# Kernel optimization log

Measured on AMD Instinct MI355X. Metric: run time of the kernel, lower is better.

The kernel has to match this reference:

```python
import jax, jax.numpy as jnp
import numpy as np

EMB = 384
HID = 256
HEADS = 4
HD = HID // HEADS  # 64
LAYERS = 2
M_DOCS = 32
TOTAL = 4096  # 1 query + 32 docs + 4063 sentences
LN_EPS = 1e-5


def _layernorm(x, scale, bias):
    mu = jnp.mean(x, axis=-1, keepdims=True)
    var = jnp.mean(jnp.square(x - mu), axis=-1, keepdims=True)
    return (x - mu) * jax.lax.rsqrt(var + LN_EPS) * scale + bias


def setup_inputs() -> dict:
    key = jax.random.key(0)
    ks = jax.random.split(key, 12)
    g = 0.05  # small init scale (stand-in for xavier)
    return {
        "node_embeddings": jax.random.normal(ks[0], (TOTAL, EMB), jnp.float32),
        "adj": jax.random.randint(ks[1], (TOTAL, TOTAL), 0, 2, jnp.int32),
        "num_docs": M_DOCS,
        "proj_w": jax.random.normal(ks[2], (HID, EMB), jnp.float32) * g,
        "proj_b": jnp.zeros((HID,), jnp.float32),
        "ln_scale": jnp.ones((LAYERS, HID), jnp.float32),
        "ln_bias": jnp.zeros((LAYERS, HID), jnp.float32),
        "gat_W": jax.random.normal(ks[3], (LAYERS, HEADS, HD, HID), jnp.float32) * g,
        "gat_a": jax.random.normal(ks[4], (LAYERS, HEADS, 2 * HD), jnp.float32) * g,
        "fusion_w": jax.random.normal(ks[5], (HID, 2 * HID + 2), jnp.float32) * g,
        "fusion_b": jnp.zeros((HID,), jnp.float32),
        "out_w": jax.random.normal(ks[6], (HID,), jnp.float32) * g,
        "out_b": jnp.float32(0.5),
    }


def reference(node_embeddings, adj, num_docs, proj_w, proj_b, ln_scale, ln_bias,
              gat_W, gat_a, fusion_w, fusion_b, out_w, out_b):
    T = node_embeddings.shape[0]
    M = num_docs
    N = T - 1 - M  # number of sentences
    # input projection + relu (dropout = identity in eval)
    h = jax.nn.relu(node_embeddings @ proj_w.T + proj_b)  # (T, HID)
    # query-guided sentence re-weighting
    q = h[0:1]                     # (1, HID)
    s = h[1 + M:]                  # (N, HID)
    qn = q / (jnp.linalg.norm(q, axis=1, keepdims=True) + 1e-8)
    sn = s / (jnp.linalg.norm(s, axis=1, keepdims=True) + 1e-8)
    cos = (qn @ sn.T).reshape(-1, 1)          # (N,1)
    s = s + 0.8 * q * cos
    h = jnp.concatenate([h[:1 + M], s], axis=0)
    mask = (adj == 0)[None]                   # (1,T,T)
    for i in range(LAYERS):
        res = h
        x = _layernorm(h, ln_scale[i], ln_bias[i])
        Wh = jnp.einsum('nd,hkd->hnk', x, gat_W[i])                # (H,T,HD)
        # concat-attention a.[Wh_i ; Wh_j] == a_src.Wh_i + a_dst.Wh_j
        src = jnp.einsum('hnk,hk->hn', Wh, gat_a[i, :, :HD])       # (H,T)
        dst = jnp.einsum('hnk,hk->hn', Wh, gat_a[i, :, HD:])       # (H,T)
        e = jax.nn.leaky_relu(src[:, :, None] + dst[:, None, :], 0.2)  # (H,T,T)
        e = jnp.where(mask, -jnp.inf, e)
        attn = jax.nn.softmax(e, axis=-1)                          # softmax over j
        hn = jnp.einsum('hij,hjk->hik', attn, Wh)                  # (H,T,HD)
        hcat = jnp.transpose(hn, (1, 0, 2)).reshape(T, HEADS * HD)
        h = 0.5 * jax.nn.relu(hcat) + 0.5 * res
    qh = h[0:1]
    sh = h[1 + M:]
    scores = (qh @ sh.T) / (HID ** 0.5)       # (1,N)
    aw = jax.nn.softmax(scores, axis=-1)
    awT = aw.T                                # (N,1)
    qw = qh * (awT + 0.5)                     # (N,HID)
    qnf = qh / (jnp.linalg.norm(qh, axis=1, keepdims=True) + 1e-8)
    snf = sh / (jnp.linalg.norm(sh, axis=1, keepdims=True) + 1e-8)
    cosf = (qnf @ snf.T).reshape(-1, 1)       # (N,1)
    feat = jnp.concatenate([sh, qw, cosf, awT], axis=1)  # (N, 2*HID+2)
    g = jax.nn.relu(feat @ fusion_w.T + fusion_b)
    out = g @ out_w + out_b                   # (N,)
    return out + 0.5 * cosf[:, 0]
```

## Files before the change

### kernel.cpp

```cpp
#include <hip/hip_runtime.h>
#include <hip/hip_bf16.h>
#include <stdint.h>

#define TOTAL 4096
#define EMB 384
#define MD 32
#define NDOCS (TOTAL - 1 - MD)
#define LN_EPS 1e-5f

typedef __hip_bfloat16 bf16;
typedef unsigned short ushort_t;
typedef __attribute__((ext_vector_type(8))) short short8;
typedef __attribute__((ext_vector_type(4))) float f32x4;
typedef __attribute__((ext_vector_type(2))) float f32x2;

__device__ __forceinline__ float ldf(const void* p, int i, int isbf) {
    return isbf ? __bfloat162float(((const bf16*)p)[i]) : ((const float*)p)[i];
}

__device__ __forceinline__ unsigned f2bf(float x) {
    return (__float_as_uint(x) + 0x8000u) >> 16;
}

__device__ __forceinline__ unsigned fenc(float f) {
    unsigned u = __float_as_uint(f);
    return (u >> 31) ? ~u : (u | 0x80000000u);
}
__device__ __forceinline__ float fdec(unsigned k) {
    return __uint_as_float((k & 0x80000000u) ? (k & 0x7FFFFFFFu) : ~k);
}

#define NTRANS ((EMB * 256 + 2 * 65536 + 514 * 256) / 256)
__global__ void k_adjmask(const int* adj, unsigned long long* maskb,
                          const uint16_t* embp, int* flag, unsigned* dmaxu,
                          const void* proj_w, const void* gat_W, const void* fusion_w,
                          float* projT, float* gatT, float* fwT) {
    __shared__ int red[4];
    int i = blockIdx.x, t = threadIdx.x;
    int w = t >> 6, l = t & 63;
    for (int c = w; c < 64; c += 4) {
        int a = adj[(size_t)i * TOTAL + c * 64 + l];
        unsigned long long m = __ballot(a != 0);
        if (l == 0) maskb[i * 64 + c] = m;
    }
    if (i == 0) {
        for (int idx = t; idx < 2048; idx += 256) dmaxu[idx] = 0x007FFFFFu;
    }
    if (i < NTRANS) {
        int cnt = 0;
        for (int k = t; k < 4096; k += 256) {
            uint16_t wd = embp[2 * k];
            int e = (wd >> 7) & 0xFF;
            if (e >= 100 && e <= 140) cnt++;
        }
        for (int o = 32; o > 0; o >>= 1) cnt += __shfl_down(cnt, o);
        if ((t & 63) == 0) red[t >> 6] = cnt;
        __syncthreads();
        int isbf = (red[0] + red[1] + red[2] + red[3] > 2048) ? 1 : 0;
        if (i == 0 && t == 0) flag[0] = isbf;
        int idx = i * 256 + t;
        if (idx < EMB * 256) {
            int d = idx >> 8, c = idx & 255;
            projT[idx] = ldf(proj_w, c * EMB + d, isbf);
        } else if (idx < EMB * 256 + 2 * 65536) {
            int r = idx - EMB * 256;
            int ll = r >> 16, rem = r & 65535;
            int d = rem >> 8, c = rem & 255;
            gatT[r] = ldf(gat_W, ll * 65536 + c * 256 + d, isbf);
        } else {
            int r = idx - (EMB * 256 + 2 * 65536);
            int j = r >> 8, c = r & 255;
            fwT[r] = ldf(fusion_w, c * 514 + j, isbf);
        }
    }
}

#define PR 8
__global__ void k_proj(const void* emb, const void* proj_b, const float* projT, float* h,
                       const int* flagp) {
    __shared__ float xs[PR][EMB];
    int isbf = flagp[0];
    int i0 = blockIdx.x * PR, t = threadIdx.x;
    for (int idx = t; idx < PR * EMB; idx += 256) {
        int r = idx / EMB, d = idx % EMB;
        xs[r][d] = ldf(emb, (i0 + r) * EMB + d, isbf);
    }
    __syncthreads();
    float acc[PR];
    float bias = ldf(proj_b, t, isbf);
#pragma unroll
    for (int r = 0; r < PR; r++) acc[r] = bias;
    for (int d0 = 0; d0 < EMB; d0 += 4) {
        float w0 = projT[d0 * 256 + t];
        float w1 = projT[(d0 + 1) * 256 + t];
        float w2 = projT[(d0 + 2) * 256 + t];
        float w3 = projT[(d0 + 3) * 256 + t];
#pragma unroll
        for (int r = 0; r < PR; r++) {
            float4 x = *(const float4*)&xs[r][d0];
            acc[r] = fmaf(x.x, w0, acc[r]);
            acc[r] = fmaf(x.y, w1, acc[r]);
            acc[r] = fmaf(x.z, w2, acc[r]);
            acc[r] = fmaf(x.w, w3, acc[r]);
        }
    }
#pragma unroll
    for (int r = 0; r < PR; r++) h[(size_t)(i0 + r) * 256 + t] = fmaxf(acc[r], 0.f);
}

#define LR 8
__global__ void k_ln_wh(float* h, const float* gatT, const void* ln_scale,
                        const void* ln_bias, const void* gat_a,
                        ushort_t* whswz, float* srcb, unsigned* d12g, unsigned* dmaxu,
                        const float* hnp, const float* lpart, int layer, int doepi,
                        const int* flagp) {
    __shared__ float xs[LR][256];
    __shared__ float red[2][LR][4];
    __shared__ float qsm[256];
    __shared__ float qred[4];
    int isbf = flagp[0];
    int i0 = blockIdx.x * LR, t = threadIdx.x;
    int w = t >> 6, l = t & 63;
    float scale = ldf(ln_scale, layer * 256 + t, isbf);
    float bias = ldf(ln_bias, layer * 256 + t, isbf);
    float hv[LR];
    if (doepi) {
#pragma unroll
        for (int r = 0; r < LR; r++) {
            int i = i0 + r;
            float lsum = lpart[(size_t)w * 4096 + i] + lpart[(size_t)(4 + w) * 4096 + i] +
                         lpart[(size_t)(8 + w) * 4096 + i] + lpart[(size_t)(12 + w) * 4096 + i];
            float s = hnp[(size_t)i * 256 + t] + hnp[(size_t)TOTAL * 256 + i * 256 + t] +
                      hnp[(size_t)2 * TOTAL * 256 + i * 256 + t] +
                      hnp[(size_t)3 * TOTAL * 256 + i * 256 + t];
            float hn = 0.5f * fmaxf(s / lsum, 0.f) + 0.5f * h[(size_t)i * 256 + t];
            hv[r] = hn;
            h[(size_t)i * 256 + t] = hn;
        }
    } else {
        qsm[t] = h[t];
#pragma unroll
        for (int r = 0; r < LR; r++) hv[r] = h[(size_t)(i0 + r) * 256 + t];
        __syncthreads();
        float qv = qsm[t];
        {
            float a = qv * qv;
            for (int o = 32; o > 0; o >>= 1) a += __shfl_down(a, o);
            if (l == 0) qred[w] = a;
        }
#pragma unroll
        for (int r = 0; r < LR; r++) {
            float b = hv[r] * hv[r], c = qv * hv[r];
            for (int o = 32; o > 0; o >>= 1) { b += __shfl_down(b, o); c += __shfl_down(c, o); }
            if (l == 0) { red[0][r][w] = b; red[1][r][w] = c; }
        }
        __syncthreads();
        if (i0 + LR > 1 + MD) {
            float qn = sqrtf(qred[0] + qred[1] + qred[2] + qred[3]) + 1e-8f;
#pragma unroll
            for (int r = 0; r < LR; r++) {
                int i = i0 + r;
                if (i >= 1 + MD) {
                    float bs = red[0][r][0] + red[0][r][1] + red[0][r][2] + red[0][r][3];
                    float cs = red[1][r][0] + red[1][r][1] + red[1][r][2] + red[1][r][3];
                    float k = 0.8f * (cs / (qn * (sqrtf(bs) + 1e-8f)));
                    hv[r] += k * qv;
                    h[(size_t)i * 256 + t] = hv[r];
                }
            }
        }
        __syncthreads();
    }
#pragma unroll
    for (int r = 0; r < LR; r++) {
        float a = hv[r], b = hv[r] * hv[r];
        for (int o = 32; o > 0; o >>= 1) { a += __shfl_down(a, o); b += __shfl_down(b, o); }
        if (l == 0) { red[0][r][w] = a; red[1][r][w] = b; }
    }
    __syncthreads();
#pragma unroll
    for (int r = 0; r < LR; r++) {
        float mu = (red[0][r][0] + red[0][r][1] + red[0][r][2] + red[0][r][3]) * (1.f / 256.f);
        float var = (red[1][r][0] + red[1][r][1] + red[1][r][2] + red[1][r][3]) * (1.f / 256.f) - mu * mu;
        float x = (hv[r] - mu) * rsqrtf(var + LN_EPS) * scale + bias;
        xs[r][t] = x;
    }
    __syncthreads();
    const float* gT = gatT + layer * 65536;
    float acc[LR];
#pragma unroll
    for (int r = 0; r < LR; r++) acc[r] = 0.f;
    for (int d0 = 0; d0 < 256; d0 += 4) {
        float w0 = gT[d0 * 256 + t];
        float w1 = gT[(d0 + 1) * 256 + t];
        float w2 = gT[(d0 + 2) * 256 + t];
        float w3 = gT[(d0 + 3) * 256 + t];
#pragma unroll
        for (int r = 0; r < LR; r++) {
            float4 x = *(const float4*)&xs[r][d0];
            acc[r] = fmaf(x.x, w0, acc[r]);
            acc[r] = fmaf(x.y, w1, acc[r]);
            acc[r] = fmaf(x.z, w2, acc[r]);
            acc[r] = fmaf(x.w, w3, acc[r]);
        }
    }
    float av1 = ldf(gat_a, layer * 512 + w * 128 + l, isbf);
    float av2 = ldf(gat_a, layer * 512 + w * 128 + 64 + l, isbf);
    const float LOG2E = 1.44269504f;
    float mmax = -__builtin_inff();
#pragma unroll
    for (int r = 0; r < LR; r++) {
        int i = i0 + r;
        int off = (i >> 6) * 16384 + (t >> 6) * 4096 + ((i >> 3) & 7) * 512 +
                  ((t >> 4) & 3) * 128 + (t & 15) * 8 + (i & 7);
        whswz[off] = (ushort_t)f2bf(acc[r]);
        float sv = acc[r] * av1, dv = acc[r] * av2;
        for (int o = 32; o > 0; o >>= 1) { sv += __shfl_down(sv, o); dv += __shfl_down(dv, o); }
        if (l == 0) {
            srcb[w * 4096 + i] = sv;
            float D1 = exp2f(dv * LOG2E), D2 = exp2f(0.2f * dv * LOG2E);
            d12g[w * 4096 + i] = (f2bf(D2) << 16) | f2bf(D1);
            mmax = fmaxf(mmax, dv);
        }
    }
    if (l == 0) atomicMax(&dmaxu[(blockIdx.x & 63) * 16 + w], fenc(mmax));
}

#define TI 32
#define JS 4
__global__ __launch_bounds__(512) void k_pv(const ushort_t* whswz, const float* srcb,
                                            const unsigned* dmaxu, const unsigned* d12g,
                                            const unsigned long long* maskb,
                                            float* hnp, float* lpart) {
    __shared__ __align__(16) char smem[32768];
    __shared__ __align__(16) float lsh[4][2][4][4];
    __shared__ unsigned mlut[4];
    __shared__ float dmx[4];
    unsigned* d12s = (unsigned*)smem;
    unsigned long long* mbs = (unsigned long long*)(smem + 16384);
    float* srcs = (float*)(smem + 16384 + 4352);
    f32x4* accsh = (f32x4*)smem;
    int t = threadIdx.x;
    int W = t >> 6, lane = t & 63;
    int h = W & 3, kq = W >> 2;
    int quad = lane >> 4, c16 = lane & 15;
    int i0 = blockIdx.x * TI;
    int jbase = blockIdx.y * 1024;
    if (t < 4) mlut[t] = (t & 1 ? 0x0000FFFFu : 0u) | (t & 2 ? 0xFFFF0000u : 0u);
    if (t < 256) {
        int hh = t >> 6, sl = t & 63;
        float v = fdec(dmaxu[sl * 16 + hh]);
        for (int o = 32; o > 0; o >>= 1) v = fmaxf(v, __shfl_xor(v, o));
        if (sl == 0) dmx[hh] = v;
    }
    for (int idx = t; idx < TI * 16; idx += 512) {
        int r = idx >> 4, wd = idx & 15;
        mbs[r * 17 + wd] = maskb[(size_t)(i0 + r) * 64 + (jbase >> 6) + wd];
    }
    for (int idx = t; idx < 1024; idx += 512) {
        int hh = idx >> 8, j4 = idx & 255;
        ((uint4*)d12s)[idx] = ((const uint4*)(d12g + hh * 4096 + jbase))[j4];
    }
    if (t < 128) {
        int h2 = t >> 5, r = t & 31;
        srcs[h2 * 32 + r] = srcb[h2 * 4096 + i0 + r];
    }
    __syncthreads();
    const float LOG2E = 1.44269504f;
    float dm = dmx[h];
    float E1[2], E2[2];
#pragma unroll
    for (int rt = 0; rt < 2; rt++) {
        float src = srcs[h * 32 + rt * 16 + c16];
        float sd = src + dm;
        float rce = -fmaxf(sd, 0.2f * sd);
        E1[rt] = exp2f((src + rce) * LOG2E);
        E2[rt] = exp2f((0.2f * src + rce) * LOG2E);
    }
    f32x4 acc[2][4];
    f32x4 accl[2] = {(f32x4){0.f, 0.f, 0.f, 0.f}, (f32x4){0.f, 0.f, 0.f, 0.f}};
#pragma unroll
    for (int rt = 0; rt < 2; rt++)
#pragma unroll
        for (int ct = 0; ct < 4; ct++) acc[rt][ct] = (f32x4){0.f, 0.f, 0.f, 0.f};
    uint4 onesu;
    unsigned os = (c16 == 0) ? 0x3F803F80u : 0u;
    onesu.x = os; onesu.y = os; onesu.z = os; onesu.w = os;
    short8 bfones = __builtin_bit_cast(short8, onesu);
    const uint4* g4 = (const uint4*)whswz;
    size_t b0 = (size_t)(jbase >> 6) * 2048 + h * 512 + (kq * 4 + quad) * 64 + c16;
    uint4 bn[4];
#pragma unroll
    for (int ct = 0; ct < 4; ct++) bn[ct] = g4[b0 + ct * 16];
    for (int step = 0; step < 16; step++) {
        uint4 bc[4];
#pragma unroll
        for (int ct = 0; ct < 4; ct++) bc[ct] = bn[ct];
        if (step < 15) {
            size_t bs = b0 + (size_t)(step + 1) * 2048;
#pragma unroll
            for (int ct = 0; ct < 4; ct++) bn[ct] = g4[bs + ct * 16];
        }
        int jl0 = step * 64 + kq * 32 + quad * 8;
        unsigned mby[2];
#pragma unroll
        for (int rt = 0; rt < 2; rt++)
            mby[rt] = (unsigned)(mbs[(rt * 16 + c16) * 17 + step] >> (kq * 32 + quad * 8)) & 0xFFu;
        const uint4* dj = (const uint4*)&d12s[h * 1024 + jl0];
        uint4 da = dj[0], db = dj[1];
        unsigned dw[8] = {da.x, da.y, da.z, da.w, db.x, db.y, db.z, db.w};
        f32x2 D1[4], D2[4];
#pragma unroll
        for (int q = 0; q < 4; q++) {
            unsigned a = dw[2 * q], b = dw[2 * q + 1];
            D1[q] = (f32x2){__uint_as_float(a << 16), __uint_as_float(b << 16)};
            D2[q] = (f32x2){__uint_as_float(a & 0xFFFF0000u), __uint_as_float(b & 0xFFFF0000u)};
        }
        uint4 afu[2];
#pragma unroll
        for (int rt = 0; rt < 2; rt++) {
            unsigned pu[4];
#pragma unroll
            for (int q = 0; q < 4; q++) {
                f32x2 v1 = D1[q] * E1[rt];
                f32x2 v2 = D2[q] * E2[rt];
                f32x2 m = __builtin_elementwise_max(v1, v2);
                unsigned v = ((__float_as_uint(m.x) + 0x8000u) >> 16) |
                             ((__float_as_uint(m.y) + 0x8000u) & 0xFFFF0000u);
                pu[q] = v & mlut[(mby[rt] >> (2 * q)) & 3u];
            }
            afu[rt].x = pu[0]; afu[rt].y = pu[1]; afu[rt].z = pu[2]; afu[rt].w = pu[3];
        }
        short8 af0 = __builtin_bit_cast(short8, afu[0]);
        short8 af1 = __builtin_bit_cast(short8, afu[1]);
#pragma unroll
        for (int ct = 0; ct < 4; ct++) {
            short8 bf = __builtin_bit_cast(short8, bc[ct]);
            acc[0][ct] = __builtin_amdgcn_mfma_f32_16x16x32_bf16(af0, bf, acc[0][ct], 0, 0, 0);
            acc[1][ct] = __builtin_amdgcn_mfma_f32_16x16x32_bf16(af1, bf, acc[1][ct], 0, 0, 0);
        }
        accl[0] = __builtin_amdgcn_mfma_f32_16x16x32_bf16(af0, bfones, accl[0], 0, 0, 0);
        accl[1] = __builtin_amdgcn_mfma_f32_16x16x32_bf16(af1, bfones, accl[1], 0, 0, 0);
    }
    __syncthreads();
    if (kq == 1) {
#pragma unroll
        for (int rt = 0; rt < 2; rt++) {
#pragma unroll
            for (int ct = 0; ct < 4; ct++)
                accsh[((h * 2 + rt) * 4 + ct) * 64 + lane] = acc[rt][ct];
            if (c16 == 0) *(f32x4*)&lsh[h][rt][quad][0] = accl[rt];
        }
    }
    __syncthreads();
    if (kq == 0) {
        float* out = hnp + (size_t)blockIdx.y * (TOTAL * 256);
#pragma unroll
        for (int rt = 0; rt < 2; rt++) {
#pragma unroll
            for (int ct = 0; ct < 4; ct++) {
                f32x4 o = acc[rt][ct] + accsh[((h * 2 + rt) * 4 + ct) * 64 + lane];
#pragma unroll
                for (int rr = 0; rr < 4; rr++) {
                    int row = i0 + rt * 16 + quad * 4 + rr;
                    out[(size_t)row * 256 + h * 64 + ct * 16 + c16] = o[rr];
                }
            }
            if (c16 == 0) {
                f32x4 lv = accl[rt] + *(const f32x4*)&lsh[h][rt][quad][0];
#pragma unroll
                for (int rr = 0; rr < 4; rr++)
                    lpart[(size_t)(blockIdx.y * 4 + h) * 4096 + i0 + rt * 16 + quad * 4 + rr] = lv[rr];
            }
        }
    }
}

__global__ __launch_bounds__(256) void k_scores(float* h, const float* hnp, const float* lpart,
                                                float* qrow, float* scoresv, float* cosv,
                                                float* swp) {
    int t = threadIdx.x, W = t >> 6, lane = t & 63;
    int hh = lane >> 4;
    float4* h4 = (float4*)h;
    const float4* p0 = (const float4*)hnp;
    const float4* p1 = p0 + (size_t)TOTAL * 64;
    const float4* p2 = p1 + (size_t)TOTAL * 64;
    const float4* p3 = p2 + (size_t)TOTAL * 64;
    int gw = blockIdx.x * 4 + W;
    float lq = lpart[(size_t)hh * 4096] + lpart[(size_t)(4 + hh) * 4096] +
               lpart[(size_t)(8 + hh) * 4096] + lpart[(size_t)(12 + hh) * 4096];
    float4 a0 = p0[lane], a1 = p1[lane], a2 = p2[lane], a3 = p3[lane];
    float4 hq = h4[lane];
    float invq = 1.f / lq;
    float4 q4;
    q4.x = 0.5f * fmaxf((a0.x + a1.x + a2.x + a3.x) * invq, 0.f) + 0.5f * hq.x;
    q4.y = 0.5f * fmaxf((a0.y + a1.y + a2.y + a3.y) * invq, 0.f) + 0.5f * hq.y;
    q4.z = 0.5f * fmaxf((a0.z + a1.z + a2.z + a3.z) * invq, 0.f) + 0.5f * hq.z;
    q4.w = 0.5f * fmaxf((a0.w + a1.w + a2.w + a3.w) * invq, 0.f) + 0.5f * hq.w;
    if (gw == 0) ((float4*)qrow)[lane] = q4;
    float a = q4.x * q4.x + q4.y * q4.y + q4.z * q4.z + q4.w * q4.w;
    for (int o = 32; o > 0; o >>= 1) a += __shfl_xor(a, o);
    float qn = sqrtf(a) + 1e-8f;
    float mw = -__builtin_inff(), sw = 0.f;
    for (int n = gw; n < NDOCS; n += 1024) {
        int row = 1 + MD + n;
        size_t ro = (size_t)row * 64;
        float ld = lpart[(size_t)hh * 4096 + row] + lpart[(size_t)(4 + hh) * 4096 + row] +
                   lpart[(size_t)(8 + hh) * 4096 + row] + lpart[(size_t)(12 + hh) * 4096 + row];
        float4 b0 = p0[ro + lane], b1 = p1[ro + lane], b2 = p2[ro + lane], b3 = p3[ro + lane];
        float4 ho = h4[ro + lane];
        float invd = 1.f / ld;
        float4 s4;
        s4.x = 0.5f * fmaxf((b0.x + b1.x + b2.x + b3.x) * invd, 0.f) + 0.5f * ho.x;
        s4.y = 0.5f * fmaxf((b0.y + b1.y + b2.y + b3.y) * invd, 0.f) + 0.5f * ho.y;
        s4.z = 0.5f * fmaxf((b0.z + b1.z + b2.z + b3.z) * invd, 0.f) + 0.5f * ho.z;
        s4.w = 0.5f * fmaxf((b0.w + b1.w + b2.w + b3.w) * invd, 0.f) + 0.5f * ho.w;
        h4[ro + lane] = s4;
        float b = s4.x * s4.x + s4.y * s4.y + s4.z * s4.z + s4.w * s4.w;
        float c = q4.x * s4.x + q4.y * s4.y + q4.z * s4.z + q4.w * s4.w;
        for (int o = 32; o > 0; o >>= 1) { b += __shfl_xor(b, o); c += __shfl_xor(c, o); }
        float sc = c * (1.f / 16.f);
        if (lane == 0) {
            scoresv[n] = sc;
            cosv[n] = c / (qn * (sqrtf(b) + 1e-8f));
        }
        float mn = fmaxf(mw, sc);
        sw = sw * __expf(mw - mn) + __expf(sc - mn);
        mw = mn;
    }
    if (lane == 0) { swp[2 * gw] = mw; swp[2 * gw + 1] = sw; }
}

#define TN 8
__global__ __launch_bounds__(256) void k_fusion(const float* h, const float* qrow,
                                                const float* scoresv, const float* swp,
                                                const float* cosv,
                                                const float* fwT, const void* fusion_b,
                                                const void* out_w, const void* out_bp,
                                                void* outv, const int* flagp) {
    __shared__ float feats2[514][TN];
    __shared__ float qhs[256];
    __shared__ float red[TN][4];
    __shared__ float reds[2][4];
    __shared__ float aws[TN];
    int isbf = flagp[0];
    int t = threadIdx.x;
    int n0 = blockIdx.x * TN;
    qhs[t] = qrow[t];
    float M = -__builtin_inff(), S = 0.f;
    for (int idx = t; idx < 1024; idx += 256) {
        float pm = swp[2 * idx], ps = swp[2 * idx + 1];
        float mn = fmaxf(M, pm);
        S = S * __expf(M - mn) + ps * __expf(pm - mn);
        M = mn;
    }
    for (int o = 32; o > 0; o >>= 1) {
        float m2 = __shfl_xor(M, o), s2 = __shfl_xor(S, o);
        float mn = fmaxf(M, m2);
        S = S * __expf(M - mn) + s2 * __expf(m2 - mn);
        M = mn;
    }
    if ((t & 63) == 0) { reds[0][t >> 6] = M; reds[1][t >> 6] = S; }
    __syncthreads();
    float Mf = fmaxf(fmaxf(reds[0][0], reds[0][1]), fmaxf(reds[0][2], reds[0][3]));
    float Sf = reds[1][0] * __expf(reds[0][0] - Mf) + reds[1][1] * __expf(reds[0][1] - Mf) +
               reds[1][2] * __expf(reds[0][2] - Mf) + reds[1][3] * __expf(reds[0][3] - Mf);
    float invS = 1.f / Sf;
    if (t < TN) {
        int n = n0 + t;
        aws[t] = (n < NDOCS) ? __expf(scoresv[n] - Mf) * invS : 0.f;
    }
    __syncthreads();
    for (int idx = t; idx < 514 * TN; idx += 256) {
        int j = idx >> 3, r = idx & 7;
        int n = n0 + r;
        float v = 0.f;
        if (n < NDOCS) {
            if (j < 256) v = h[(size_t)(1 + MD + n) * 256 + j];
            else if (j < 512) v = qhs[j - 256] * (aws[r] + 0.5f);
            else if (j == 512) v = cosv[n];
            else v = aws[r];
        }
        feats2[j][r] = v;
    }
    __syncthreads();
    float acc[TN];
    float bk = ldf(fusion_b, t, isbf);
#pragma unroll
    for (int r = 0; r < TN; r++) acc[r] = bk;
    for (int j0 = 0; j0 < 512; j0 += 8) {
        float wv[8];
#pragma unroll
        for (int u = 0; u < 8; u++) wv[u] = fwT[(j0 + u) * 256 + t];
#pragma unroll
        for (int u = 0; u < 8; u++) {
            float4 fa = *(const float4*)&feats2[j0 + u][0];
            float4 fb = *(const float4*)&feats2[j0 + u][4];
            acc[0] = fmaf(fa.x, wv[u], acc[0]); acc[1] = fmaf(fa.y, wv[u], acc[1]);
            acc[2] = fmaf(fa.z, wv[u], acc[2]); acc[3] = fmaf(fa.w, wv[u], acc[3]);
            acc[4] = fmaf(fb.x, wv[u], acc[4]); acc[5] = fmaf(fb.y, wv[u], acc[5]);
            acc[6] = fmaf(fb.z, wv[u], acc[6]); acc[7] = fmaf(fb.w, wv[u], acc[7]);
        }
    }
#pragma unroll
    for (int j = 512; j < 514; j++) {
        float wv = fwT[j * 256 + t];
#pragma unroll
        for (int r = 0; r < TN; r++) acc[r] = fmaf(feats2[j][r], wv, acc[r]);
    }
    float ow = ldf(out_w, t, isbf);
    float outb = ldf(out_bp, 0, isbf);
#pragma unroll
    for (int r = 0; r < TN; r++) {
        float o = fmaxf(acc[r], 0.f) * ow;
        for (int off = 32; off > 0; off >>= 1) o += __shfl_down(o, off);
        if ((t & 63) == 0) red[r][t >> 6] = o;
    }
    __syncthreads();
    if (t < TN) {
        int n = n0 + t;
        if (n < NDOCS) {
            float o = red[t][0] + red[t][1] + red[t][2] + red[t][3] + outb + 0.5f * cosv[n];
            if (isbf) ((bf16*)outv)[n] = __float2bfloat16(o);
            else      ((float*)outv)[n] = o;
        }
    }
}

extern "C" void kernel_launch(void* const* d_in, const int* in_sizes, int n_in,
                              void* d_out, int out_size, void* d_ws, size_t ws_size,
                              hipStream_t stream) {
    const void* emb      = d_in[0];
    const int*  adj      = (const int*)d_in[1];
    const void* proj_w   = d_in[3];
    const void* proj_b   = d_in[4];
    const void* ln_scale = d_in[5];
    const void* ln_bias  = d_in[6];
    const void* gat_W    = d_in[7];
    const void* gat_a    = d_in[8];
    const void* fusion_w = d_in[9];
    const void* fusion_b = d_in[10];
    const void* out_w    = d_in[11];
    const void* out_b    = d_in[12];

    unsigned long long* maskb = (unsigned long long*)d_ws;
    int* flag = (int*)((char*)d_ws + (size_t)4096 * 64 * 8);
    float* f = (float*)((char*)d_ws + (size_t)4096 * 64 * 8 + 256);
    float* h       = f; f += 4096 * 256;
    float* srcb    = f; f += 4 * 4096;
    unsigned* d12g = (unsigned*)f; f += 4 * 4096;
    unsigned* dmaxu = (unsigned*)f; f += 2048;
    float* projT   = f; f += EMB * 256;
    float* gatT    = f; f += 2 * 65536;
    float* fwT     = f; f += 514 * 256;
    float* scoresv = f; f += 4096;
    float* cosv    = f; f += 4096;
    float* swpart  = f; f += 4096;
    float* qrow    = f; f += 256;
    float* lpart   = f; f += 4 * 4 * 4096;
    ushort_t* whswz = (ushort_t*)f; f += 4096 * 256 / 2;
    float* hnp     = f; f += (size_t)JS * 4096 * 256;

    k_adjmask<<<dim3(4096), dim3(256), 0, stream>>>(adj, maskb, (const uint16_t*)emb, flag,
                                                    dmaxu, proj_w, gat_W, fusion_w,
                                                    projT, gatT, fwT);
    k_proj<<<dim3(TOTAL / PR), dim3(256), 0, stream>>>(emb, proj_b, projT, h, flag);
    for (int layer = 0; layer < 2; layer++) {
        k_ln_wh<<<dim3(TOTAL / LR), dim3(256), 0, stream>>>(h, gatT, ln_scale, ln_bias, gat_a,
                                                            whswz, srcb, d12g, dmaxu + layer * 1024,
                                                            hnp, lpart, layer, layer, flag);
        k_pv<<<dim3(TOTAL / TI, JS), dim3(512), 0, stream>>>(whswz, srcb, dmaxu + layer * 1024,
                                                             d12g, maskb, hnp, lpart);
    }
    k_scores<<<dim3(256), dim3(256), 0, stream>>>(h, hnp, lpart, qrow, scoresv, cosv, swpart);
    k_fusion<<<dim3((NDOCS + TN - 1) / TN), dim3(256), 0, stream>>>(h, qrow, scoresv, swpart,
                                                                    cosv, fwT, fusion_b, out_w,
                                                                    out_b, (void*)d_out, flag);
}
```

Baseline: 304.1 us.

## Fuse projection, GAT layers, scoring and fusion into one persistent kernel

Replaces the chain of seven kernel launches after the mask build with one persistent kernel of 512 blocks of 512 threads. The stages are separated by software grid barriers built from atomics, and dynamic shared memory is reused across stages. The aim is to remove launch overhead and inter-kernel gaps. In exchange, stages that used 256 threads leave half of each block idle, the barriers rely on all blocks being co-resident, and the spin loop has a timeout fallback that could break correctness.

```diff
diff --git a/kernel.cpp b/kernel.cpp
--- a/kernel.cpp
+++ b/kernel.cpp
@@ -7,6 +7,7 @@
 #define MD 32
 #define NDOCS (TOTAL - 1 - MD)
 #define LN_EPS 1e-5f
+#define NEGF (-1e30f)
 
 typedef __hip_bfloat16 bf16;
 typedef unsigned short ushort_t;
@@ -30,11 +31,30 @@
     return __uint_as_float((k & 0x80000000u) ? (k & 0x7FFFFFFFu) : ~k);
 }
 
+__device__ __forceinline__ void gsync(unsigned* bar) {
+    __syncthreads();
+    if (threadIdx.x == 0) {
+        __threadfence();
+        unsigned old = atomicAdd(bar, 1u);
+        if (old == 511u) {
+            __hip_atomic_store(bar + 32, 1u, __ATOMIC_RELEASE, __HIP_MEMORY_SCOPE_AGENT);
+        } else {
+            long long t0 = clock64();
+            while (__hip_atomic_load(bar + 32, __ATOMIC_ACQUIRE, __HIP_MEMORY_SCOPE_AGENT) == 0u) {
+                __builtin_amdgcn_s_sleep(8);
+                if (clock64() - t0 > 200000000LL) break;
+            }
+        }
+    }
+    __syncthreads();
+    __threadfence();
+}
+
 #define NTRANS ((EMB * 256 + 2 * 65536 + 514 * 256) / 256)
 __global__ void k_adjmask(const int* adj, unsigned long long* maskb,
                           const uint16_t* embp, int* flag, unsigned* dmaxu,
                           const void* proj_w, const void* gat_W, const void* fusion_w,
-                          float* projT, float* gatT, float* fwT) {
+                          float* projT, float* gatT, float* fwT, unsigned* gbar) {
     __shared__ int red[4];
     int i = blockIdx.x, t = threadIdx.x;
     int w = t >> 6, l = t & 63;
@@ -45,6 +65,7 @@
     }
     if (i == 0) {
         for (int idx = t; idx < 2048; idx += 256) dmaxu[idx] = 0x007FFFFFu;
+        for (int idx = t; idx < 384; idx += 256) gbar[idx] = 0u;
     }
     if (i < NTRANS) {
         int cnt = 0;
@@ -76,86 +97,101 @@
 }
 
 #define PR 8
-__global__ void k_proj(const void* emb, const void* proj_b, const float* projT, float* h,
-                       const int* flagp) {
-    __shared__ float xs[PR][EMB];
-    int isbf = flagp[0];
-    int i0 = blockIdx.x * PR, t = threadIdx.x;
-    for (int idx = t; idx < PR * EMB; idx += 256) {
-        int r = idx / EMB, d = idx % EMB;
-        xs[r][d] = ldf(emb, (i0 + r) * EMB + d, isbf);
-    }
-    __syncthreads();
-    float acc[PR];
-    float bias = ldf(proj_b, t, isbf);
-#pragma unroll
-    for (int r = 0; r < PR; r++) acc[r] = bias;
-    for (int d0 = 0; d0 < EMB; d0 += 4) {
-        float w0 = projT[d0 * 256 + t];
-        float w1 = projT[(d0 + 1) * 256 + t];
-        float w2 = projT[(d0 + 2) * 256 + t];
-        float w3 = projT[(d0 + 3) * 256 + t];
-#pragma unroll
-        for (int r = 0; r < PR; r++) {
-            float4 x = *(const float4*)&xs[r][d0];
-            acc[r] = fmaf(x.x, w0, acc[r]);
-            acc[r] = fmaf(x.y, w1, acc[r]);
-            acc[r] = fmaf(x.z, w2, acc[r]);
-            acc[r] = fmaf(x.w, w3, acc[r]);
-        }
-    }
-#pragma unroll
-    for (int r = 0; r < PR; r++) h[(size_t)(i0 + r) * 256 + t] = fmaxf(acc[r], 0.f);
+__device__ __forceinline__ void dev_proj(const void* emb, const void* proj_b,
+                                         const float* projT, float* h, int isbf, int bid) {
+    extern __shared__ char BIGDYN[];
+    float (*xs)[EMB] = (float (*)[EMB])BIGDYN;
+    int t5 = threadIdx.x;
+    bool act = t5 < 256;
+    int t = t5 & 255;
+    int i0 = bid * PR;
+    if (act) {
+        for (int idx = t; idx < PR * EMB; idx += 256) {
+            int r = idx / EMB, d = idx % EMB;
+            xs[r][d] = ldf(emb, (i0 + r) * EMB + d, isbf);
+        }
+    }
+    __syncthreads();
+    if (act) {
+        float acc[PR];
+        float bias = ldf(proj_b, t, isbf);
+#pragma unroll
+        for (int r = 0; r < PR; r++) acc[r] = bias;
+        for (int d0 = 0; d0 < EMB; d0 += 4) {
+            float w0 = projT[d0 * 256 + t];
+            float w1 = projT[(d0 + 1) * 256 + t];
+            float w2 = projT[(d0 + 2) * 256 + t];
+            float w3 = projT[(d0 + 3) * 256 + t];
+#pragma unroll
+            for (int r = 0; r < PR; r++) {
+                float4 x = *(const float4*)&xs[r][d0];
+                acc[r] = fmaf(x.x, w0, acc[r]);
+                acc[r] = fmaf(x.y, w1, acc[r]);
+                acc[r] = fmaf(x.z, w2, acc[r]);
+                acc[r] = fmaf(x.w, w3, acc[r]);
+            }
+        }
+#pragma unroll
+        for (int r = 0; r < PR; r++) h[(size_t)(i0 + r) * 256 + t] = fmaxf(acc[r], 0.f);
+    }
 }
 
 #define LR 8
-__global__ void k_ln_wh(float* h, const float* gatT, const void* ln_scale,
-                        const void* ln_bias, const void* gat_a,
-                        ushort_t* whswz, float* srcb, unsigned* d12g, unsigned* dmaxu,
-                        const float* hnp, const float* lpart, int layer, int doepi,
-                        const int* flagp) {
-    __shared__ float xs[LR][256];
+__device__ __forceinline__ void dev_ln(float* h, const float* gatT, const void* ln_scale,
+        const void* ln_bias, const void* gat_a, ushort_t* whswz, float* srcb,
+        unsigned* d12g, unsigned* dmaxu, const float* hnp, const float* lpart,
+        int layer, int doepi, int isbf, int bid) {
+    extern __shared__ char BIGDYN[];
+    float (*xs)[256] = (float (*)[256])BIGDYN;
     __shared__ float red[2][LR][4];
     __shared__ float qsm[256];
     __shared__ float qred[4];
-    int isbf = flagp[0];
-    int i0 = blockIdx.x * LR, t = threadIdx.x;
+    int t5 = threadIdx.x;
+    bool act = t5 < 256;
+    int t = t5 & 255;
     int w = t >> 6, l = t & 63;
+    int i0 = bid * LR;
     float scale = ldf(ln_scale, layer * 256 + t, isbf);
     float bias = ldf(ln_bias, layer * 256 + t, isbf);
     float hv[LR];
+#pragma unroll
+    for (int r = 0; r < LR; r++) hv[r] = 0.f;
     if (doepi) {
-#pragma unroll
-        for (int r = 0; r < LR; r++) {
-            int i = i0 + r;
-            float lsum = lpart[(size_t)w * 4096 + i] + lpart[(size_t)(4 + w) * 4096 + i] +
-                         lpart[(size_t)(8 + w) * 4096 + i] + lpart[(size_t)(12 + w) * 4096 + i];
-            float s = hnp[(size_t)i * 256 + t] + hnp[(size_t)TOTAL * 256 + i * 256 + t] +
-                      hnp[(size_t)2 * TOTAL * 256 + i * 256 + t] +
-                      hnp[(size_t)3 * TOTAL * 256 + i * 256 + t];
-            float hn = 0.5f * fmaxf(s / lsum, 0.f) + 0.5f * h[(size_t)i * 256 + t];
-            hv[r] = hn;
-            h[(size_t)i * 256 + t] = hn;
+        if (act) {
+#pragma unroll
+            for (int r = 0; r < LR; r++) {
+                int i = i0 + r;
+                float lsum = lpart[(size_t)w * 4096 + i] + lpart[(size_t)(4 + w) * 4096 + i] +
+                             lpart[(size_t)(8 + w) * 4096 + i] + lpart[(size_t)(12 + w) * 4096 + i];
+                float s = hnp[(size_t)i * 256 + t] + hnp[(size_t)TOTAL * 256 + i * 256 + t] +
+                          hnp[(size_t)2 * TOTAL * 256 + i * 256 + t] +
+                          hnp[(size_t)3 * TOTAL * 256 + i * 256 + t];
+                float hn = 0.5f * fmaxf(s / lsum, 0.f) + 0.5f * h[(size_t)i * 256 + t];
+                hv[r] = hn;
+                h[(size_t)i * 256 + t] = hn;
+            }
         }
     } else {
-        qsm[t] = h[t];
-#pragma unroll
-        for (int r = 0; r < LR; r++) hv[r] = h[(size_t)(i0 + r) * 256 + t];
+        if (act) {
+            qsm[t] = h[t];
+#pragma unroll
+            for (int r = 0; r < LR; r++) hv[r] = h[(size_t)(i0 + r) * 256 + t];
+        }
         __syncthreads();
         float qv = qsm[t];
-        {
+        if (act) {
             float a = qv * qv;
             for (int o = 32; o > 0; o >>= 1) a += __shfl_down(a, o);
             if (l == 0) qred[w] = a;
-        }
-#pragma unroll
-        for (int r = 0; r < LR; r++) {
-            float b = hv[r] * hv[r], c = qv * hv[r];
-            for (int o = 32; o > 0; o >>= 1) { b += __shfl_down(b, o); c += __shfl_down(c, o); }
-            if (l == 0) { red[0][r][w] = b; red[1][r][w] = c; }
+#pragma unroll
+            for (int r = 0; r < LR; r++) {
+                float b = hv[r] * hv[r], c = qv * hv[r];
+                for (int o = 32; o > 0; o >>= 1) { b += __shfl_down(b, o); c += __shfl_down(c, o); }
+                if (l == 0) { red[0][r][w] = b; red[1][r][w] = c; }
+            }
         }
         __syncthreads();
-        if (i0 + LR > 1 + MD) {
+        if (act && i0 + LR > 1 + MD) {
             float qn = sqrtf(qred[0] + qred[1] + qred[2] + qred[3]) + 1e-8f;
 #pragma unroll
             for (int r = 0; r < LR; r++) {
@@ -171,68 +207,75 @@
         }
         __syncthreads();
     }
-#pragma unroll
-    for (int r = 0; r < LR; r++) {
-        float a = hv[r], b = hv[r] * hv[r];
-        for (int o = 32; o > 0; o >>= 1) { a += __shfl_down(a, o); b += __shfl_down(b, o); }
-        if (l == 0) { red[0][r][w] = a; red[1][r][w] = b; }
-    }
-    __syncthreads();
-#pragma unroll
-    for (int r = 0; r < LR; r++) {
-        float mu = (red[0][r][0] + red[0][r][1] + red[0][r][2] + red[0][r][3]) * (1.f / 256.f);
-        float var = (red[1][r][0] + red[1][r][1] + red[1][r][2] + red[1][r][3]) * (1.f / 256.f) - mu * mu;
-        float x = (hv[r] - mu) * rsqrtf(var + LN_EPS) * scale + bias;
-        xs[r][t] = x;
-    }
-    __syncthreads();
-    const float* gT = gatT + layer * 65536;
-    float acc[LR];
-#pragma unroll
-    for (int r = 0; r < LR; r++) acc[r] = 0.f;
-    for (int d0 = 0; d0 < 256; d0 += 4) {
-        float w0 = gT[d0 * 256 + t];
-        float w1 = gT[(d0 + 1) * 256 + t];
-        float w2 = gT[(d0 + 2) * 256 + t];
-        float w3 = gT[(d0 + 3) * 256 + t];
+    if (act) {
 #pragma unroll
         for (int r = 0; r < LR; r++) {
-            float4 x = *(const float4*)&xs[r][d0];
-            acc[r] = fmaf(x.x, w0, acc[r]);
-            acc[r] = fmaf(x.y, w1, acc[r]);
-            acc[r] = fmaf(x.z, w2, acc[r]);
-            acc[r] = fmaf(x.w, w3, acc[r]);
-        }
-    }
-    float av1 = ldf(gat_a, layer * 512 + w * 128 + l, isbf);
-    float av2 = ldf(gat_a, layer * 512 + w * 128 + 64 + l, isbf);
-    const float LOG2E = 1.44269504f;
-    float mmax = -__builtin_inff();
-#pragma unroll
-    for (int r = 0; r < LR; r++) {
-        int i = i0 + r;
-        int off = (i >> 6) * 16384 + (t >> 6) * 4096 + ((i >> 3) & 7) * 512 +
-                  ((t >> 4) & 3) * 128 + (t & 15) * 8 + (i & 7);
-        whswz[off] = (ushort_t)f2bf(acc[r]);
-        float sv = acc[r] * av1, dv = acc[r] * av2;
-        for (int o = 32; o > 0; o >>= 1) { sv += __shfl_down(sv, o); dv += __shfl_down(dv, o); }
-        if (l == 0) {
-            srcb[w * 4096 + i] = sv;
-            float D1 = exp2f(dv * LOG2E), D2 = exp2f(0.2f * dv * LOG2E);
-            d12g[w * 4096 + i] = (f2bf(D2) << 16) | f2bf(D1);
-            mmax = fmaxf(mmax, dv);
-        }
-    }
-    if (l == 0) atomicMax(&dmaxu[(blockIdx.x & 63) * 16 + w], fenc(mmax));
+            float a = hv[r], b = hv[r] * hv[r];
+            for (int o = 32; o > 0; o >>= 1) { a += __shfl_down(a, o); b += __shfl_down(b, o); }
+            if (l == 0) { red[0][r][w] = a; red[1][r][w] = b; }
+        }
+    }
+    __syncthreads();
+    if (act) {
+#pragma unroll
+        for (int r = 0; r < LR; r++) {
+            float mu = (red[0][r][0] + red[0][r][1] + red[0][r][2] + red[0][r][3]) * (1.f / 256.f);
+            float var = (red[1][r][0] + red[1][r][1] + red[1][r][2] + red[1][r][3]) * (1.f / 256.f) - mu * mu;
+            float x = (hv[r] - mu) * rsqrtf(var + LN_EPS) * scale + bias;
+            xs[r][t] = x;
+        }
+    }
+    __syncthreads();
+    if (act) {
+        const float* gT = gatT + layer * 65536;
+        float acc[LR];
+#pragma unroll
+        for (int r = 0; r < LR; r++) acc[r] = 0.f;
+        for (int d0 = 0; d0 < 256; d0 += 4) {
+            float w0 = gT[d0 * 256 + t];
+            float w1 = gT[(d0 + 1) * 256 + t];
+            float w2 = gT[(d0 + 2) * 256 + t];
+            float w3 = gT[(d0 + 3) * 256 + t];
+#pragma unroll
+            for (int r = 0; r < LR; r++) {
+                float4 x = *(const float4*)&xs[r][d0];
+                acc[r] = fmaf(x.x, w0, acc[r]);
+                acc[r] = fmaf(x.y, w1, acc[r]);
+                acc[r] = fmaf(x.z, w2, acc[r]);
+                acc[r] = fmaf(x.w, w3, acc[r]);
+            }
+        }
+        float av1 = ldf(gat_a, layer * 512 + w * 128 + l, isbf);
+        float av2 = ldf(gat_a, layer * 512 + w * 128 + 64 + l, isbf);
+        const float LOG2E = 1.44269504f;
+        float mmax = -__builtin_inff();
+#pragma unroll
+        for (int r = 0; r < LR; r++) {
+            int i = i0 + r;
+            int off = (i >> 6) * 16384 + (t >> 6) * 4096 + ((i >> 3) & 7) * 512 +
+                      ((t >> 4) & 3) * 128 + (t & 15) * 8 + (i & 7);
+            whswz[off] = (ushort_t)f2bf(acc[r]);
+            float sv = acc[r] * av1, dv = acc[r] * av2;
+            for (int o = 32; o > 0; o >>= 1) { sv += __shfl_down(sv, o); dv += __shfl_down(dv, o); }
+            if (l == 0) {
+                srcb[w * 4096 + i] = sv;
+                float D1 = exp2f(dv * LOG2E), D2 = exp2f(0.2f * dv * LOG2E);
+                d12g[w * 4096 + i] = (f2bf(D2) << 16) | f2bf(D1);
+                mmax = fmaxf(mmax, dv);
+            }
+        }
+        if (l == 0) atomicMax(&dmaxu[(bid & 63) * 16 + w], fenc(mmax));
+    }
 }
 
 #define TI 32
 #define JS 4
-__global__ __launch_bounds__(512) void k_pv(const ushort_t* whswz, const float* srcb,
-                                            const unsigned* dmaxu, const unsigned* d12g,
-                                            const unsigned long long* maskb,
-                                            float* hnp, float* lpart) {
-    __shared__ __align__(16) char smem[32768];
+__device__ __forceinline__ void dev_pv(const ushort_t* whswz, const float* srcb,
+                                       const unsigned* dmaxu, const unsigned* d12g,
+                                       const unsigned long long* maskb,
+                                       float* hnp, float* lpart, int bx, int by) {
+    extern __shared__ char BIGDYN[];
+    char* smem = BIGDYN;
     __shared__ __align__(16) float lsh[4][2][4][4];
     __shared__ unsigned mlut[4];
     __shared__ float dmx[4];
@@ -244,8 +287,8 @@
     int W = t >> 6, lane = t & 63;
     int h = W & 3, kq = W >> 2;
     int quad = lane >> 4, c16 = lane & 15;
-    int i0 = blockIdx.x * TI;
-    int jbase = blockIdx.y * 1024;
+    int i0 = bx * TI;
+    int jbase = by * 1024;
     if (t < 4) mlut[t] = (t & 1 ? 0x0000FFFFu : 0u) | (t & 2 ? 0xFFFF0000u : 0u);
     if (t < 256) {
         int hh = t >> 6, sl = t & 63;
@@ -354,7 +397,7 @@
     }
     __syncthreads();
     if (kq == 0) {
-        float* out = hnp + (size_t)blockIdx.y * (TOTAL * 256);
+        float* out = hnp + (size_t)by * (TOTAL * 256);
 #pragma unroll
         for (int rt = 0; rt < 2; rt++) {
 #pragma unroll
@@ -370,23 +413,22 @@
                 f32x4 lv = accl[rt] + *(const f32x4*)&lsh[h][rt][quad][0];
 #pragma unroll
                 for (int rr = 0; rr < 4; rr++)
-                    lpart[(size_t)(blockIdx.y * 4 + h) * 4096 + i0 + rt * 16 + quad * 4 + rr] = lv[rr];
-            }
-        }
-    }
-}
-
-__global__ __launch_bounds__(256) void k_scores(float* h, const float* hnp, const float* lpart,
-                                                float* qrow, float* scoresv, float* cosv,
-                                                float* swp) {
-    int t = threadIdx.x, W = t >> 6, lane = t & 63;
+                    lpart[(size_t)(by * 4 + h) * 4096 + i0 + rt * 16 + quad * 4 + rr] = lv[rr];
+            }
+        }
+    }
+}
+
+__device__ __forceinline__ void dev_scores(float* h, const float* hnp, const float* lpart,
+                                           float* qrow, float* scoresv, float* cosv,
+                                           float* swp, int gw) {
+    int t = threadIdx.x, lane = t & 63;
     int hh = lane >> 4;
     float4* h4 = (float4*)h;
     const float4* p0 = (const float4*)hnp;
     const float4* p1 = p0 + (size_t)TOTAL * 64;
     const float4* p2 = p1 + (size_t)TOTAL * 64;
     const float4* p3 = p2 + (size_t)TOTAL * 64;
-    int gw = blockIdx.x * 4 + W;
     float lq = lpart[(size_t)hh * 4096] + lpart[(size_t)(4 + hh) * 4096] +
                lpart[(size_t)(8 + hh) * 4096] + lpart[(size_t)(12 + hh) * 4096];
     float4 a0 = p0[lane], a1 = p1[lane], a2 = p2[lane], a3 = p3[lane];
@@ -401,8 +443,8 @@
     float a = q4.x * q4.x + q4.y * q4.y + q4.z * q4.z + q4.w * q4.w;
     for (int o = 32; o > 0; o >>= 1) a += __shfl_xor(a, o);
     float qn = sqrtf(a) + 1e-8f;
-    float mw = -__builtin_inff(), sw = 0.f;
-    for (int n = gw; n < NDOCS; n += 1024) {
+    float mw = NEGF, sw = 0.f;
+    for (int n = gw; n < NDOCS; n += 4096) {
         int row = 1 + MD + n;
         size_t ro = (size_t)row * 64;
         float ld = lpart[(size_t)hh * 4096 + row] + lpart[(size_t)(4 + hh) * 4096 + row] +
@@ -432,99 +474,134 @@
 }
 
 #define TN 8
-__global__ __launch_bounds__(256) void k_fusion(const float* h, const float* qrow,
-                                                const float* scoresv, const float* swp,
-                                                const float* cosv,
-                                                const float* fwT, const void* fusion_b,
-                                                const void* out_w, const void* out_bp,
-                                                void* outv, const int* flagp) {
-    __shared__ float feats2[514][TN];
+__device__ __forceinline__ void dev_fusion(const float* h, const float* qrow,
+                                           const float* scoresv, const float* swp,
+                                           const float* cosv, const float* fwT,
+                                           const void* fusion_b, const void* out_w,
+                                           const void* out_bp, void* outv, int isbf, int bid) {
+    extern __shared__ char BIGDYN[];
+    float (*feats2)[TN] = (float (*)[TN])BIGDYN;
     __shared__ float qhs[256];
-    __shared__ float red[TN][4];
+    __shared__ float redf[TN][4];
     __shared__ float reds[2][4];
     __shared__ float aws[TN];
-    int isbf = flagp[0];
-    int t = threadIdx.x;
-    int n0 = blockIdx.x * TN;
-    qhs[t] = qrow[t];
-    float M = -__builtin_inff(), S = 0.f;
-    for (int idx = t; idx < 1024; idx += 256) {
-        float pm = swp[2 * idx], ps = swp[2 * idx + 1];
-        float mn = fmaxf(M, pm);
-        S = S * __expf(M - mn) + ps * __expf(pm - mn);
-        M = mn;
-    }
-    for (int o = 32; o > 0; o >>= 1) {
-        float m2 = __shfl_xor(M, o), s2 = __shfl_xor(S, o);
-        float mn = fmaxf(M, m2);
-        S = S * __expf(M - mn) + s2 * __expf(m2 - mn);
-        M = mn;
-    }
-    if ((t & 63) == 0) { reds[0][t >> 6] = M; reds[1][t >> 6] = S; }
+    int t5 = threadIdx.x;
+    bool act = t5 < 256;
+    int t = t5 & 255;
+    int n0 = bid * TN;
+    if (act) qhs[t] = qrow[t];
+    float M = NEGF, S = 0.f;
+    if (act) {
+        for (int idx = t; idx < 4096; idx += 256) {
+            float pm = swp[2 * idx], ps = swp[2 * idx + 1];
+            float mn = fmaxf(M, pm);
+            S = S * __expf(M - mn) + ps * __expf(pm - mn);
+            M = mn;
+        }
+        for (int o = 32; o > 0; o >>= 1) {
+            float m2 = __shfl_xor(M, o), s2 = __shfl_xor(S, o);
+            float mn = fmaxf(M, m2);
+            S = S * __expf(M - mn) + s2 * __expf(m2 - mn);
+            M = mn;
+        }
+        if ((t & 63) == 0) { reds[0][t >> 6] = M; reds[1][t >> 6] = S; }
+    }
     __syncthreads();
     float Mf = fmaxf(fmaxf(reds[0][0], reds[0][1]), fmaxf(reds[0][2], reds[0][3]));
     float Sf = reds[1][0] * __expf(reds[0][0] - Mf) + reds[1][1] * __expf(reds[0][1] - Mf) +
                reds[1][2] * __expf(reds[0][2] - Mf) + reds[1][3] * __expf(reds[0][3] - Mf);
     float invS = 1.f / Sf;
-    if (t < TN) {
-        int n = n0 + t;
-        aws[t] = (n < NDOCS) ? __expf(scoresv[n] - Mf) * invS : 0.f;
-    }
-    __syncthreads();
-    for (int idx = t; idx < 514 * TN; idx += 256) {
-        int j = idx >> 3, r = idx & 7;
-        int n = n0 + r;
-        float v = 0.f;
+    if (t5 < TN) {
+        int n = n0 + t5;
+        aws[t5] = (n < NDOCS) ? __expf(scoresv[n] - Mf) * invS : 0.f;
+    }
+    __syncthreads();
+    if (act) {
+        for (int idx = t; idx < 514 * TN; idx += 256) {
+            int j = idx >> 3, r = idx & 7;
+            int n = n0 + r;
+            float v = 0.f;
+            if (n < NDOCS) {
+                if (j < 256) v = h[(size_t)(1 + MD + n) * 256 + j];
+                else if (j < 512) v = qhs[j - 256] * (aws[r] + 0.5f);
+                else if (j == 512) v = cosv[n];
+                else v = aws[r];
+            }
+            feats2[j][r] = v;
+        }
+    }
+    __syncthreads();
+    if (act) {
+        float acc[TN];
+        float bk = ldf(fusion_b, t, isbf);
+#pragma unroll
+        for (int r = 0; r < TN; r++) acc[r] = bk;
+        for (int j0 = 0; j0 < 512; j0 += 8) {
+            float wv[8];
+#pragma unroll
+            for (int u = 0; u < 8; u++) wv[u] = fwT[(j0 + u) * 256 + t];
+#pragma unroll
+            for (int u = 0; u < 8; u++) {
+                float4 fa = *(const float4*)&feats2[j0 + u][0];
+                float4 fb = *(const float4*)&feats2[j0 + u][4];
+                acc[0] = fmaf(fa.x, wv[u], acc[0]); acc[1] = fmaf(fa.y, wv[u], acc[1]);
+                acc[2] = fmaf(fa.z, wv[u], acc[2]); acc[3] = fmaf(fa.w, wv[u], acc[3]);
+                acc[4] = fmaf(fb.x, wv[u], acc[4]); acc[5] = fmaf(fb.y, wv[u], acc[5]);
+                acc[6] = fmaf(fb.z, wv[u], acc[6]); acc[7] = fmaf(fb.w, wv[u], acc[7]);
+            }
+        }
+#pragma unroll
+        for (int j = 512; j < 514; j++) {
+            float wv = fwT[j * 256 + t];
+#pragma unroll
+            for (int r = 0; r < TN; r++) acc[r] = fmaf(feats2[j][r], wv, acc[r]);
+        }
+        float ow = ldf(out_w, t, isbf);
+#pragma unroll
+        for (int r = 0; r < TN; r++) {
+            float o = fmaxf(acc[r], 0.f) * ow;
+            for (int off = 32; off > 0; off >>= 1) o += __shfl_down(o, off);
+            if ((t & 63) == 0) redf[r][t >> 6] = o;
+        }
+    }
+    __syncthreads();
+    if (t5 < TN) {
+        int n = n0 + t5;
         if (n < NDOCS) {
-            if (j < 256) v = h[(size_t)(1 + MD + n) * 256 + j];
-            else if (j < 512) v = qhs[j - 256] * (aws[r] + 0.5f);
-            else if (j == 512) v = cosv[n];
-            else v = aws[r];
-        }
-        feats2[j][r] = v;
-    }
-    __syncthreads();
-    float acc[TN];
-    float bk = ldf(fusion_b, t, isbf);
-#pragma unroll
-    for (int r = 0; r < TN; r++) acc[r] = bk;
-    for (int j0 = 0; j0 < 512; j0 += 8) {
-        float wv[8];
-#pragma unroll
-        for (int u = 0; u < 8; u++) wv[u] = fwT[(j0 + u) * 256 + t];
-#pragma unroll
-        for (int u = 0; u < 8; u++) {
-            float4 fa = *(const float4*)&feats2[j0 + u][0];
-            float4 fb = *(const float4*)&feats2[j0 + u][4];
-            acc[0] = fmaf(fa.x, wv[u], acc[0]); acc[1] = fmaf(fa.y, wv[u], acc[1]);
-            acc[2] = fmaf(fa.z, wv[u], acc[2]); acc[3] = fmaf(fa.w, wv[u], acc[3]);
-            acc[4] = fmaf(fb.x, wv[u], acc[4]); acc[5] = fmaf(fb.y, wv[u], acc[5]);
-            acc[6] = fmaf(fb.z, wv[u], acc[6]); acc[7] = fmaf(fb.w, wv[u], acc[7]);
-        }
-    }
-#pragma unroll
-    for (int j = 512; j < 514; j++) {
-        float wv = fwT[j * 256 + t];
-#pragma unroll
-        for (int r = 0; r < TN; r++) acc[r] = fmaf(feats2[j][r], wv, acc[r]);
-    }
-    float ow = ldf(out_w, t, isbf);
-    float outb = ldf(out_bp, 0, isbf);
-#pragma unroll
-    for (int r = 0; r < TN; r++) {
-        float o = fmaxf(acc[r], 0.f) * ow;
-        for (int off = 32; off > 0; off >>= 1) o += __shfl_down(o, off);
-        if ((t & 63) == 0) red[r][t >> 6] = o;
-    }
-    __syncthreads();
-    if (t < TN) {
-        int n = n0 + t;
-        if (n < NDOCS) {
-            float o = red[t][0] + red[t][1] + red[t][2] + red[t][3] + outb + 0.5f * cosv[n];
+            float outb = ldf(out_bp, 0, isbf);
+            float o = redf[t5][0] + redf[t5][1] + redf[t5][2] + redf[t5][3] + outb + 0.5f * cosv[n];
             if (isbf) ((bf16*)outv)[n] = __float2bfloat16(o);
             else      ((float*)outv)[n] = o;
         }
     }
+}
+
+__global__ __launch_bounds__(512, 4) void k_mega(
+        const void* emb, const void* proj_b, const float* projT, float* h,
+        const float* gatT, const void* ln_scale, const void* ln_bias, const void* gat_a,
+        ushort_t* whswz, float* srcb, unsigned* d12g, unsigned* dmaxu,
+        const unsigned long long* maskb, float* hnp, float* lpart,
+        float* qrow, float* scoresv, float* cosv, float* swp,
+        const float* fwT, const void* fusion_b, const void* out_w, const void* out_bp,
+        void* outv, const int* flagp, unsigned* gbar) {
+    int isbf = flagp[0];
+    int bid = blockIdx.x;
+    dev_proj(emb, proj_b, projT, h, isbf, bid);
+    gsync(gbar + 0 * 64);
+    dev_ln(h, gatT, ln_scale, ln_bias, gat_a, whswz, srcb, d12g, dmaxu, hnp, lpart,
+           0, 0, isbf, bid);
+    gsync(gbar + 1 * 64);
+    dev_pv(whswz, srcb, dmaxu, d12g, maskb, hnp, lpart, bid & 127, bid >> 7);
+    gsync(gbar + 2 * 64);
+    dev_ln(h, gatT, ln_scale, ln_bias, gat_a, whswz, srcb, d12g, dmaxu + 1024, hnp, lpart,
+           1, 1, isbf, bid);
+    gsync(gbar + 3 * 64);
+    dev_pv(whswz, srcb, dmaxu + 1024, d12g, maskb, hnp, lpart, bid & 127, bid >> 7);
+    gsync(gbar + 4 * 64);
+    dev_scores(h, hnp, lpart, qrow, scoresv, cosv, swp, bid * 8 + (threadIdx.x >> 6));
+    gsync(gbar + 5 * 64);
+    if (bid < (NDOCS + TN - 1) / TN)
+        dev_fusion(h, qrow, scoresv, swp, cosv, fwT, fusion_b, out_w, out_bp, outv, isbf, bid);
 }
 
 extern "C" void kernel_launch(void* const* d_in, const int* in_sizes, int n_in,
@@ -550,12 +627,13 @@
     float* srcb    = f; f += 4 * 4096;
     unsigned* d12g = (unsigned*)f; f += 4 * 4096;
     unsigned* dmaxu = (unsigned*)f; f += 2048;
+    unsigned* gbar = (unsigned*)f; f += 384;
     float* projT   = f; f += EMB * 256;
     float* gatT    = f; f += 2 * 65536;
     float* fwT     = f; f += 514 * 256;
     float* scoresv = f; f += 4096;
     float* cosv    = f; f += 4096;
-    float* swpart  = f; f += 4096;
+    float* swpart  = f; f += 8192;
     float* qrow    = f; f += 256;
     float* lpart   = f; f += 4 * 4 * 4096;
     ushort_t* whswz = (ushort_t*)f; f += 4096 * 256 / 2;
@@ -563,17 +641,11 @@
 
     k_adjmask<<<dim3(4096), dim3(256), 0, stream>>>(adj, maskb, (const uint16_t*)emb, flag,
                                                     dmaxu, proj_w, gat_W, fusion_w,
-                                                    projT, gatT, fwT);
-    k_proj<<<dim3(TOTAL / PR), dim3(256), 0, stream>>>(emb, proj_b, projT, h, flag);
-    for (int layer = 0; layer < 2; layer++) {
-        k_ln_wh<<<dim3(TOTAL / LR), dim3(256), 0, stream>>>(h, gatT, ln_scale, ln_bias, gat_a,
-                                                            whswz, srcb, d12g, dmaxu + layer * 1024,
-                                                            hnp, lpart, layer, layer, flag);
-        k_pv<<<dim3(TOTAL / TI, JS), dim3(512), 0, stream>>>(whswz, srcb, dmaxu + layer * 1024,
-                                                             d12g, maskb, hnp, lpart);
-    }
-    k_scores<<<dim3(256), dim3(256), 0, stream>>>(h, hnp, lpart, qrow, scoresv, cosv, swpart);
-    k_fusion<<<dim3((NDOCS + TN - 1) / TN), dim3(256), 0, stream>>>(h, qrow, scoresv, swpart,
-                                                                    cosv, fwT, fusion_b, out_w,
-                                                                    out_b, (void*)d_out, flag);
-}
+                                                    projT, gatT, fwT, gbar);
+    k_mega<<<dim3(512), dim3(512), 32768, stream>>>(emb, proj_b, projT, h, gatT,
+                                                    ln_scale, ln_bias, gat_a, whswz, srcb,
+                                                    d12g, dmaxu, maskb, hnp, lpart,
+                                                    qrow, scoresv, cosv, swpart, fwT,
+                                                    fusion_b, out_w, out_b, (void*)d_out,
+                                                    flag, gbar);
+}
```

Result: slower. 920.4 us (+202.6%).
